# Performance work log

Hardware: AMD Instinct MI355X
Metric: run time of the kernel (lower is better)

Reference implementation:

```python
import jax, jax.numpy as jnp
import numpy as np

B, S, D, H, F = 8, 1024, 1024, 16, 4096
DH = D // H
EPS = 1e-8
NEG_INF = -1e30


def setup_inputs() -> dict:
    key = jax.random.key(0)
    ks = jax.random.split(key, 12)
    x = jax.random.normal(ks[0], (B, S, D), jnp.float32)
    # variable valid lengths in [S//2, S]; True = keep (valid token)
    lengths = jax.random.randint(ks[1], (B,), S // 2, S + 1)
    src_key_padding_mask = jnp.arange(S)[None, :] < lengths[:, None]
    rel_pos_bias = 0.02 * jax.random.normal(ks[2], (1, H, S, S), jnp.float32)
    w = lambda k, sh, std: std * jax.random.normal(k, sh, jnp.float32)
    std = D ** -0.5
    return {
        'x': x,
        'src_key_padding_mask': src_key_padding_mask,
        'rel_pos_bias': rel_pos_bias,
        'Wq': w(ks[3], (D, D), std),
        'Wk': w(ks[4], (D, D), std),
        'Wv': w(ks[5], (D, D), std),
        'Wo': w(ks[6], (D, D), std),
        'g1': jnp.ones((D,), jnp.float32),
        'g2': jnp.ones((D,), jnp.float32),
        'W1': w(ks[7], (D, F), std),
        'b1': jnp.zeros((F,), jnp.float32),
        'W2': w(ks[8], (F, F and D), F ** -0.5),
        'b2': jnp.zeros((D,), jnp.float32),
    }


def rmsnorm(x, g):
    # x / sqrt(mean(x^2) + eps) * g   (no mean subtraction)
    ms = jnp.mean(x * x, axis=-1, keepdims=True)
    return x * jax.lax.rsqrt(ms + EPS) * g


def attention(h, kpm, rel_pos_bias, Wq, Wk, Wv, Wo):
    b, s, d = h.shape
    q = (h @ Wq).reshape(b, s, H, DH)
    k = (h @ Wk).reshape(b, s, H, DH)
    v = (h @ Wv).reshape(b, s, H, DH)
    scores = jnp.einsum('bqhd,bkhd->bhqk', q, k) / np.sqrt(DH)
    scores = scores + rel_pos_bias
    scores = jnp.where(kpm[:, None, None, :], scores, NEG_INF)
    attn = jax.nn.softmax(scores, axis=-1)
    out = jnp.einsum('bhqk,bkhd->bqhd', attn, v).reshape(b, s, d)
    return out @ Wo


def reference(x, src_key_padding_mask, rel_pos_bias,
              Wq, Wk, Wv, Wo, g1, g2, W1, b1, W2, b2):
    h = rmsnorm(x, g1)
    x = x + attention(h, src_key_padding_mask, rel_pos_bias, Wq, Wk, Wv, Wo)
    h = rmsnorm(x, g2)
    ff = jax.nn.relu(h @ W1 + b1) @ W2 + b2
    return x + ff
```

## Files before the change

kernel.cpp:

```cpp
#include <hip/hip_runtime.h>
#include <stdint.h>

typedef __bf16 bf16;
typedef __bf16 bf16x4 __attribute__((ext_vector_type(4)));
typedef __bf16 bf16x8 __attribute__((ext_vector_type(8)));
typedef float f32x4 __attribute__((ext_vector_type(4)));

constexpr int Bz = 8, S = 1024, D = 1024, NH = 16, DH = 64, F = 4096;

__device__ __forceinline__ bool is_f32(const uint16_t* dt) { return dt[0] == 0; }

__device__ __forceinline__ void ld4(const void* p, size_t idx, bool f32, float o[4]) {
  if (f32) {
    float4 v = *(const float4*)((const float*)p + idx);
    o[0] = v.x; o[1] = v.y; o[2] = v.z; o[3] = v.w;
  } else {
    bf16x4 v = *(const bf16x4*)((const bf16*)p + idx);
    o[0] = v[0]; o[1] = v[1]; o[2] = v[2]; o[3] = v[3];
  }
}

__device__ __forceinline__ float ld1(const void* p, size_t idx, bool f32) {
  return f32 ? ((const float*)p)[idx] : (float)((const bf16*)p)[idx];
}

__device__ __forceinline__ void gload_lds16(const bf16* g, bf16* l) {
  __builtin_amdgcn_global_load_lds(
      (const __attribute__((address_space(1))) void*)g,
      (__attribute__((address_space(3))) void*)l, 16, 0, 0);
}

__global__ void lengths_kernel(const unsigned char* __restrict__ mask,
                               int* __restrict__ lengths) {
  int b = blockIdx.x;
  int esz = (mask[1] == 1) ? 1 : ((mask[1] != 0) ? 2 : 4);
  int cnt = 0;
  for (int s = threadIdx.x; s < S; s += blockDim.x) {
    const unsigned char* p = mask + ((size_t)b * S + s) * esz;
    unsigned v = 0;
    for (int j = 0; j < esz; j++) v |= p[j];
    cnt += (v != 0) ? 1 : 0;
  }
#pragma unroll
  for (int m = 32; m >= 1; m >>= 1) cnt += __shfl_xor(cnt, m);
  __shared__ int sred[4];
  if ((threadIdx.x & 63) == 0) sred[threadIdx.x >> 6] = cnt;
  __syncthreads();
  if (threadIdx.x == 0) lengths[b] = sred[0] + sred[1] + sred[2] + sred[3];
}

__global__ void transpose_any(const void* __restrict__ src, bf16* __restrict__ dst,
                              int R, int C, const uint16_t* __restrict__ dt) {
  bool f32 = is_f32(dt);
  __shared__ bf16 tile[64][65];
  int c0 = blockIdx.x * 64, r0 = blockIdx.y * 64;
  int tx = threadIdx.x, ty = threadIdx.y;
#pragma unroll
  for (int i = 0; i < 4; i++) {
    int r = ty * 4 + i;
    float v[4];
    ld4(src, (size_t)(r0 + r) * C + c0 + tx * 4, f32, v);
#pragma unroll
    for (int j = 0; j < 4; j++) tile[r][tx * 4 + j] = (bf16)v[j];
  }
  __syncthreads();
#pragma unroll
  for (int i = 0; i < 4; i++) {
    int rr = ty * 4 + i;
    bf16x4 ov;
#pragma unroll
    for (int j = 0; j < 4; j++) ov[j] = tile[tx * 4 + j][rr];
    *(bf16x4*)(dst + (size_t)(c0 + rr) * R + r0 + tx * 4) = ov;
  }
}

__global__ void bias_cvt(const void* __restrict__ src, bf16* __restrict__ dst,
                         const uint16_t* __restrict__ dt) {
  bool f32 = is_f32(dt);
  size_t i = ((size_t)blockIdx.x * 256 + threadIdx.x) * 4;
  float v[4];
  ld4(src, i, f32, v);
  bf16x4 o;
#pragma unroll
  for (int j = 0; j < 4; j++) o[j] = (bf16)v[j];
  *(bf16x4*)(dst + i) = o;
}

template <bool ADD>
__global__ void rmsnorm_kernel(const void* __restrict__ xv, const bf16* __restrict__ add,
                               const void* __restrict__ gv, bf16* __restrict__ y,
                               const uint16_t* __restrict__ dt) {
  bool f32 = is_f32(dt);
  int row = blockIdx.x, t = threadIdx.x;
  float xf[4];
  ld4(xv, (size_t)row * D + t * 4, f32, xf);
  if (ADD) {
    bf16x4 a = *(const bf16x4*)(add + (size_t)row * D + t * 4);
#pragma unroll
    for (int j = 0; j < 4; j++) xf[j] += (float)a[j];
  }
  float ss = xf[0] * xf[0] + xf[1] * xf[1] + xf[2] * xf[2] + xf[3] * xf[3];
#pragma unroll
  for (int m = 32; m >= 1; m >>= 1) ss += __shfl_xor(ss, m);
  __shared__ float sred[4];
  if ((t & 63) == 0) sred[t >> 6] = ss;
  __syncthreads();
  float tot = sred[0] + sred[1] + sred[2] + sred[3];
  float scale = rsqrtf(tot * (1.0f / D) + 1e-8f);
  float gf[4];
  ld4(gv, (size_t)t * 4, f32, gf);
  bf16x4 ov;
#pragma unroll
  for (int j = 0; j < 4; j++) ov[j] = (bf16)(xf[j] * scale * gf[j]);
  *(bf16x4*)(y + (size_t)row * D + t * 4) = ov;
}

template <bool BIAS, bool RELU, bool RES1, bool RES2, bool OUTEXT, bool VT>
__global__ void gemm_nt(const bf16* __restrict__ A, const bf16* __restrict__ Bt,
                        void* __restrict__ Cv, const void* __restrict__ biasv,
                        const void* __restrict__ res1, const bf16* __restrict__ res2,
                        int M, int N, int K, const uint16_t* __restrict__ dt) {
  bool f32 = is_f32(dt);
  __shared__ bf16 As[2 * 4096];
  __shared__ bf16 Bs[2 * 4096];
  const int tid = threadIdx.x, lane = tid & 63, w = tid >> 6;
  const int wm = w >> 1, wn = w & 1;
  const int lid = blockIdx.x;
  const int bm = ((lid & 7) << 3) + ((lid >> 3) & 7);
  const int bn = lid >> 6;
  const int quad = lane >> 4, c = lane & 15;

  f32x4 acc[4][4];
#pragma unroll
  for (int i = 0; i < 4; i++)
#pragma unroll
    for (int j = 0; j < 4; j++)
#pragma unroll
      for (int r = 0; r < 4; r++) acc[i][j][r] = 0.f;

  const bf16* gA = A + (size_t)(bm * 128 + w * 16 + (lane >> 2)) * K + (lane & 3) * 8;
  const bf16* gB = Bt + (size_t)(bn * 128 + w * 16 + (lane >> 2)) * K + (lane & 3) * 8;
  bf16* lA = As + w * 512;
  bf16* lB = Bs + w * 512;
  const size_t rstep = (size_t)64 * K;

  int aoff[4], boff[4];
#pragma unroll
  for (int i = 0; i < 4; i++) {
    aoff[i] = (wm * 64 + i * 16 + c) * 32 + quad * 8;
    boff[i] = (wn * 64 + i * 16 + c) * 32 + quad * 8;
  }

  for (int k0 = 0; k0 < K; k0 += 64) {
    __syncthreads();
#pragma unroll
    for (int p = 0; p < 2; p++) {
      gload_lds16(gA + p * 32, lA + p * 4096);
      gload_lds16(gA + p * 32 + rstep, lA + p * 4096 + 2048);
      gload_lds16(gB + p * 32, lB + p * 4096);
      gload_lds16(gB + p * 32 + rstep, lB + p * 4096 + 2048);
    }
    gA += 64;
    gB += 64;
    __syncthreads();
#pragma unroll
    for (int p = 0; p < 2; p++) {
      bf16x8 af[4], bfr[4];
#pragma unroll
      for (int i = 0; i < 4; i++) af[i] = *(const bf16x8*)(As + p * 4096 + aoff[i]);
#pragma unroll
      for (int i = 0; i < 4; i++) bfr[i] = *(const bf16x8*)(Bs + p * 4096 + boff[i]);
#pragma unroll
      for (int i = 0; i < 4; i++)
#pragma unroll
        for (int j = 0; j < 4; j++)
          acc[i][j] = __builtin_amdgcn_mfma_f32_16x16x32_bf16(af[i], bfr[j], acc[i][j], 0, 0, 0);
    }
  }

  const int m0 = bm * 128 + wm * 64, n0 = bn * 128 + wn * 64;
#pragma unroll
  for (int i = 0; i < 4; i++) {
#pragma unroll
    for (int j = 0; j < 4; j++) {
      int col = n0 + j * 16 + c;
      if (VT) {
        int row0 = m0 + i * 16 + quad * 4;
        int bb = row0 >> 10, s0 = row0 & 1023;
        int hh = col >> 6, dd = col & 63;
        bf16x4 ov;
#pragma unroll
        for (int r = 0; r < 4; r++) ov[r] = (bf16)acc[i][j][r];
        *(bf16x4*)((bf16*)Cv + ((size_t)((bb << 4) + hh) * 64 + dd) * 1024 + s0) = ov;
      } else {
        float bv = BIAS ? ld1(biasv, col, f32) : 0.f;
#pragma unroll
        for (int r = 0; r < 4; r++) {
          int row = m0 + i * 16 + quad * 4 + r;
          size_t idx = (size_t)row * N + col;
          float vv = acc[i][j][r] + bv;
          if (RELU) vv = fmaxf(vv, 0.f);
          if (RES1) vv += ld1(res1, idx, f32);
          if (RES2) vv += (float)res2[idx];
          if (OUTEXT && f32) ((float*)Cv)[idx] = vv;
          else ((bf16*)Cv)[idx] = (bf16)vv;
        }
      }
    }
  }
}

__global__ void __launch_bounds__(256) attn_kernel(
    const bf16* __restrict__ qk, const bf16* __restrict__ vt,
    const bf16* __restrict__ bias, const int* __restrict__ lengths,
    bf16* __restrict__ out) {
  __shared__ bf16 Qs[64][72];
  __shared__ bf16 Ks[64][72];
  __shared__ bf16 Vs[64][72];
  __shared__ bf16 Ps[4][16][72];
  const int tid = threadIdx.x, lane = tid & 63, w = tid >> 6;
  const int id = blockIdx.x;
  const int qt = id >> 7, b = (id >> 4) & 7, h = id & 15;
  const int len = lengths[b];
  const int quad = lane >> 4, c = lane & 15;
  const int r4 = tid >> 2, c4 = tid & 3;

  {
    size_t qrow = (size_t)(b * S + qt * 64 + r4) * 2048 + h * 64 + c4 * 8;
    *(bf16x8*)&Qs[r4][c4 * 8] = *(const bf16x8*)&qk[qrow];
    *(bf16x8*)&Qs[r4][32 + c4 * 8] = *(const bf16x8*)&qk[qrow + 32];
  }
  __syncthreads();
  const bf16x8 a0 = *(const bf16x8*)&Qs[w * 16 + c][quad * 8];
  const bf16x8 a1 = *(const bf16x8*)&Qs[w * 16 + c][32 + quad * 8];

  float l_[4] = {0.f, 0.f, 0.f, 0.f};
  f32x4 o[4];
#pragma unroll
  for (int ni = 0; ni < 4; ni++)
#pragma unroll
    for (int r = 0; r < 4; r++) o[ni][r] = 0.f;

  const bf16* bb = bias + (size_t)h * S * S + (size_t)(qt * 64 + w * 16 + quad * 4) * S;
  const int nkt = (len + 63) >> 6;

  for (int kt = 0; kt < nkt; kt++) {
    __syncthreads();
    {
      size_t krow = (size_t)(b * S + kt * 64 + r4) * 2048 + 1024 + h * 64 + c4 * 8;
      *(bf16x8*)&Ks[r4][c4 * 8] = *(const bf16x8*)&qk[krow];
      *(bf16x8*)&Ks[r4][32 + c4 * 8] = *(const bf16x8*)&qk[krow + 32];
      size_t vrow = ((size_t)((b * 16 + h) * 64 + r4)) * 1024 + kt * 64 + c4 * 8;
      *(bf16x8*)&Vs[r4][c4 * 8] = *(const bf16x8*)&vt[vrow];
      *(bf16x8*)&Vs[r4][32 + c4 * 8] = *(const bf16x8*)&vt[vrow + 32];
    }
    __syncthreads();

    f32x4 s[4];
#pragma unroll
    for (int ni = 0; ni < 4; ni++)
#pragma unroll
      for (int r = 0; r < 4; r++) s[ni][r] = 0.f;
#pragma unroll
    for (int ni = 0; ni < 4; ni++) {
      bf16x8 b0 = *(const bf16x8*)&Ks[ni * 16 + c][quad * 8];
      bf16x8 b1 = *(const bf16x8*)&Ks[ni * 16 + c][32 + quad * 8];
      s[ni] = __builtin_amdgcn_mfma_f32_16x16x32_bf16(a0, b0, s[ni], 0, 0, 0);
      s[ni] = __builtin_amdgcn_mfma_f32_16x16x32_bf16(a1, b1, s[ni], 0, 0, 0);
    }

    const bool full = (kt * 64 + 64 <= len);
#pragma unroll
    for (int ni = 0; ni < 4; ni++) {
      int col = kt * 64 + ni * 16 + c;
      bool valid = full || (col < len);
#pragma unroll
      for (int r = 0; r < 4; r++) {
        float vb = (float)bb[(size_t)r * S + col];
        float p = valid ? __expf(s[ni][r] * 0.125f + vb) : 0.f;
        s[ni][r] = p;
        l_[r] += p;
      }
    }

#pragma unroll
    for (int ni = 0; ni < 4; ni++)
#pragma unroll
      for (int r = 0; r < 4; r++) Ps[w][quad * 4 + r][ni * 16 + c] = (bf16)s[ni][r];

    bf16x8 p0 = *(const bf16x8*)&Ps[w][c][quad * 8];
    bf16x8 p1 = *(const bf16x8*)&Ps[w][c][32 + quad * 8];
#pragma unroll
    for (int ni = 0; ni < 4; ni++) {
      bf16x8 vb0 = *(const bf16x8*)&Vs[ni * 16 + c][quad * 8];
      bf16x8 vb1 = *(const bf16x8*)&Vs[ni * 16 + c][32 + quad * 8];
      o[ni] = __builtin_amdgcn_mfma_f32_16x16x32_bf16(p0, vb0, o[ni], 0, 0, 0);
      o[ni] = __builtin_amdgcn_mfma_f32_16x16x32_bf16(p1, vb1, o[ni], 0, 0, 0);
    }
  }

  float inv[4];
#pragma unroll
  for (int r = 0; r < 4; r++) {
    float l = l_[r];
    l += __shfl_xor(l, 1);
    l += __shfl_xor(l, 2);
    l += __shfl_xor(l, 4);
    l += __shfl_xor(l, 8);
    inv[r] = 1.f / l;
  }
#pragma unroll
  for (int ni = 0; ni < 4; ni++)
#pragma unroll
    for (int r = 0; r < 4; r++) {
      size_t idx = ((size_t)(b * S + qt * 64 + w * 16 + quad * 4 + r)) * D + h * 64 + ni * 16 + c;
      out[idx] = (bf16)(o[ni][r] * inv[r]);
    }
}

extern "C" void kernel_launch(void* const* d_in, const int* in_sizes, int n_in,
                              void* d_out, int out_size, void* d_ws, size_t ws_size,
                              hipStream_t stream) {
  const void* x = d_in[0];
  const unsigned char* mask = (const unsigned char*)d_in[1];
  const void* rpb = d_in[2];
  const void* Wq = d_in[3];
  const void* Wk = d_in[4];
  const void* Wv = d_in[5];
  const void* Wo = d_in[6];
  const void* g1 = d_in[7];
  const void* g2 = d_in[8];
  const void* W1 = d_in[9];
  const void* b1 = d_in[10];
  const void* W2 = d_in[11];
  const void* b2 = d_in[12];
  const uint16_t* dt = (const uint16_t*)d_in[7];

  char* ws = (char*)d_ws;
  const size_t MB = 1024 * 1024;
  bf16* WqkT = (bf16*)(ws + 0 * MB);
  bf16* WkT = (bf16*)(ws + 2 * MB);
  bf16* WvT = (bf16*)(ws + 4 * MB);
  bf16* WoT = (bf16*)(ws + 6 * MB);
  bf16* W1T = (bf16*)(ws + 8 * MB);
  bf16* W2T = (bf16*)(ws + 16 * MB);
  bf16* hbuf = (bf16*)(ws + 24 * MB);
  bf16* qkbuf = (bf16*)(ws + 40 * MB);
  bf16* d1buf = (bf16*)(ws + 40 * MB);
  bf16* vtbuf = (bf16*)(ws + 72 * MB);
  bf16* biasb = (bf16*)(ws + 88 * MB);
  bf16* a1b = (bf16*)(ws + 56 * MB);
  int* lens = (int*)d_out;

  dim3 tb(16, 16);
  lengths_kernel<<<dim3(8), dim3(256), 0, stream>>>(mask, lens);
  transpose_any<<<dim3(16, 16), tb, 0, stream>>>(Wq, WqkT, 1024, 1024, dt);
  transpose_any<<<dim3(16, 16), tb, 0, stream>>>(Wk, WkT, 1024, 1024, dt);
  transpose_any<<<dim3(16, 16), tb, 0, stream>>>(Wv, WvT, 1024, 1024, dt);
  transpose_any<<<dim3(16, 16), tb, 0, stream>>>(Wo, WoT, 1024, 1024, dt);
  transpose_any<<<dim3(64, 16), tb, 0, stream>>>(W1, W1T, 1024, 4096, dt);
  transpose_any<<<dim3(16, 64), tb, 0, stream>>>(W2, W2T, 4096, 1024, dt);
  bias_cvt<<<dim3(16384), dim3(256), 0, stream>>>(rpb, biasb, dt);

  rmsnorm_kernel<false><<<dim3(8192), dim3(256), 0, stream>>>(x, nullptr, g1, hbuf, dt);
  gemm_nt<false, false, false, false, false, false><<<dim3(16 * 64), dim3(256), 0, stream>>>(
      hbuf, WqkT, qkbuf, nullptr, nullptr, nullptr, 8192, 2048, 1024, dt);
  gemm_nt<false, false, false, false, false, true><<<dim3(8 * 64), dim3(256), 0, stream>>>(
      hbuf, WvT, vtbuf, nullptr, nullptr, nullptr, 8192, 1024, 1024, dt);
  attn_kernel<<<dim3(2048), dim3(256), 0, stream>>>(qkbuf, vtbuf, biasb, lens, hbuf);
  gemm_nt<false, false, false, false, false, false><<<dim3(8 * 64), dim3(256), 0, stream>>>(
      hbuf, WoT, d1buf, nullptr, nullptr, nullptr, 8192, 1024, 1024, dt);
  rmsnorm_kernel<true><<<dim3(8192), dim3(256), 0, stream>>>(x, d1buf, g2, hbuf, dt);
  gemm_nt<true, true, false, false, false, false><<<dim3(32 * 64), dim3(256), 0, stream>>>(
      hbuf, W1T, a1b, b1, nullptr, nullptr, 8192, 4096, 1024, dt);
  gemm_nt<true, false, true, true, true, false><<<dim3(8 * 64), dim3(256), 0, stream>>>(
      a1b, W2T, d_out, b2, x, d1buf, 8192, 1024, 4096, dt);

  (void)in_sizes; (void)n_in; (void)out_size; (void)ws_size;
}
```

Before: 586.5 us.

## Load Q/K/V MFMA fragments directly from global memory, dropping shared-memory staging

The attention kernel no longer stages Q, K and V tiles through LDS with block-wide barriers. Each wave now loads its MFMA operand fragments straight from global memory into registers, and V is fetched early to overlap with the softmax. This removes the __syncthreads and LDS round trips per key tile. In exchange, the four waves each re-read the same K/V data from global/L2 (4x redundant traffic) with less coalesced 16-byte row-strided accesses, and register pressure goes up.

```diff
diff --git a/kernel.cpp b/kernel.cpp
--- a/kernel.cpp
+++ b/kernel.cpp
@@ -214,25 +214,16 @@
     const bf16* __restrict__ qk, const bf16* __restrict__ vt,
     const bf16* __restrict__ bias, const int* __restrict__ lengths,
     bf16* __restrict__ out) {
-  __shared__ bf16 Qs[64][72];
-  __shared__ bf16 Ks[64][72];
-  __shared__ bf16 Vs[64][72];
   __shared__ bf16 Ps[4][16][72];
   const int tid = threadIdx.x, lane = tid & 63, w = tid >> 6;
   const int id = blockIdx.x;
   const int qt = id >> 7, b = (id >> 4) & 7, h = id & 15;
   const int len = lengths[b];
   const int quad = lane >> 4, c = lane & 15;
-  const int r4 = tid >> 2, c4 = tid & 3;
-
-  {
-    size_t qrow = (size_t)(b * S + qt * 64 + r4) * 2048 + h * 64 + c4 * 8;
-    *(bf16x8*)&Qs[r4][c4 * 8] = *(const bf16x8*)&qk[qrow];
-    *(bf16x8*)&Qs[r4][32 + c4 * 8] = *(const bf16x8*)&qk[qrow + 32];
-  }
-  __syncthreads();
-  const bf16x8 a0 = *(const bf16x8*)&Qs[w * 16 + c][quad * 8];
-  const bf16x8 a1 = *(const bf16x8*)&Qs[w * 16 + c][32 + quad * 8];
+
+  const size_t qbase = (size_t)(b * S + qt * 64 + w * 16 + c) * 2048 + h * 64 + quad * 8;
+  const bf16x8 a0 = *(const bf16x8*)&qk[qbase];
+  const bf16x8 a1 = *(const bf16x8*)&qk[qbase + 32];
 
   float l_[4] = {0.f, 0.f, 0.f, 0.f};
   f32x4 o[4];
@@ -242,20 +233,18 @@
     for (int r = 0; r < 4; r++) o[ni][r] = 0.f;
 
   const bf16* bb = bias + (size_t)h * S * S + (size_t)(qt * 64 + w * 16 + quad * 4) * S;
+  const bf16* kbase = qk + (size_t)b * S * 2048 + 1024 + h * 64 + quad * 8;
+  const bf16* vbase = vt + ((size_t)((b * 16 + h) * 64) + c) * 1024 + quad * 8;
   const int nkt = (len + 63) >> 6;
 
   for (int kt = 0; kt < nkt; kt++) {
-    __syncthreads();
-    {
-      size_t krow = (size_t)(b * S + kt * 64 + r4) * 2048 + 1024 + h * 64 + c4 * 8;
-      *(bf16x8*)&Ks[r4][c4 * 8] = *(const bf16x8*)&qk[krow];
-      *(bf16x8*)&Ks[r4][32 + c4 * 8] = *(const bf16x8*)&qk[krow + 32];
-      size_t vrow = ((size_t)((b * 16 + h) * 64 + r4)) * 1024 + kt * 64 + c4 * 8;
-      *(bf16x8*)&Vs[r4][c4 * 8] = *(const bf16x8*)&vt[vrow];
-      *(bf16x8*)&Vs[r4][32 + c4 * 8] = *(const bf16x8*)&vt[vrow + 32];
-    }
-    __syncthreads();
-
+    bf16x8 kf0[4], kf1[4];
+#pragma unroll
+    for (int ni = 0; ni < 4; ni++) {
+      const bf16* kr = kbase + (size_t)(kt * 64 + ni * 16 + c) * 2048;
+      kf0[ni] = *(const bf16x8*)kr;
+      kf1[ni] = *(const bf16x8*)(kr + 32);
+    }
     f32x4 s[4];
 #pragma unroll
     for (int ni = 0; ni < 4; ni++)
@@ -263,10 +252,16 @@
       for (int r = 0; r < 4; r++) s[ni][r] = 0.f;
 #pragma unroll
     for (int ni = 0; ni < 4; ni++) {
-      bf16x8 b0 = *(const bf16x8*)&Ks[ni * 16 + c][quad * 8];
-      bf16x8 b1 = *(const bf16x8*)&Ks[ni * 16 + c][32 + quad * 8];
-      s[ni] = __builtin_amdgcn_mfma_f32_16x16x32_bf16(a0, b0, s[ni], 0, 0, 0);
-      s[ni] = __builtin_amdgcn_mfma_f32_16x16x32_bf16(a1, b1, s[ni], 0, 0, 0);
+      s[ni] = __builtin_amdgcn_mfma_f32_16x16x32_bf16(a0, kf0[ni], s[ni], 0, 0, 0);
+      s[ni] = __builtin_amdgcn_mfma_f32_16x16x32_bf16(a1, kf1[ni], s[ni], 0, 0, 0);
+    }
+
+    bf16x8 vf0[4], vf1[4];
+#pragma unroll
+    for (int ni = 0; ni < 4; ni++) {
+      const bf16* vr = vbase + (size_t)(ni * 16) * 1024 + kt * 64;
+      vf0[ni] = *(const bf16x8*)vr;
+      vf1[ni] = *(const bf16x8*)(vr + 32);
     }
 
     const bool full = (kt * 64 + 64 <= len);
@@ -292,10 +287,8 @@
     bf16x8 p1 = *(const bf16x8*)&Ps[w][c][32 + quad * 8];
 #pragma unroll
     for (int ni = 0; ni < 4; ni++) {
-      bf16x8 vb0 = *(const bf16x8*)&Vs[ni * 16 + c][quad * 8];
-      bf16x8 vb1 = *(const bf16x8*)&Vs[ni * 16 + c][32 + quad * 8];
-      o[ni] = __builtin_amdgcn_mfma_f32_16x16x32_bf16(p0, vb0, o[ni], 0, 0, 0);
-      o[ni] = __builtin_amdgcn_mfma_f32_16x16x32_bf16(p1, vb1, o[ni], 0, 0, 0);
+      o[ni] = __builtin_amdgcn_mfma_f32_16x16x32_bf16(p0, vf0[ni], o[ni], 0, 0, 0);
+      o[ni] = __builtin_amdgcn_mfma_f32_16x16x32_bf16(p1, vf1[ni], o[ni], 0, 0, 0);
     }
   }
 
```

Result: slower. 716.5 us (+22.2%).
